# Kernel optimization log

Measured on AMD Instinct MI355X. Metric: run time of the kernel, lower is better.

## Reference

```python
import jax, jax.numpy as jnp
import numpy as np

N_HIDDEN = 14  # number of interior Linear(50,50)+ReLU layers (16 Linears total)
WIDTH = 50
IN_DIM = 16
OUT_DIM = 4
BATCH = 2_000_000


def setup_inputs() -> dict:
    key = jax.random.key(0)
    ks = jax.random.split(key, 7)
    s_in = 1.0 / np.sqrt(IN_DIM)
    s_h = 1.0 / np.sqrt(WIDTH)
    x = jax.random.normal(ks[0], (BATCH, IN_DIM), dtype=jnp.float32)
    W0 = jax.random.uniform(ks[1], (WIDTH, IN_DIM), jnp.float32, -s_in, s_in)
    b0 = jax.random.uniform(ks[2], (WIDTH,), jnp.float32, -s_in, s_in)
    Wh = jax.random.uniform(ks[3], (N_HIDDEN, WIDTH, WIDTH), jnp.float32, -s_h, s_h)
    bh = jax.random.uniform(ks[4], (N_HIDDEN, WIDTH), jnp.float32, -s_h, s_h)
    Wo = jax.random.uniform(ks[5], (OUT_DIM, WIDTH), jnp.float32, -s_h, s_h)
    bo = jax.random.uniform(ks[6], (OUT_DIM,), jnp.float32, -s_h, s_h)
    return {"x": x, "W0": W0, "b0": b0, "Wh": Wh, "bh": bh, "Wo": Wo, "bo": bo}


def reference(x, W0, b0, Wh, bh, Wo, bo):
    # first layer: Linear(in,50) + ReLU   (torch Linear: y = x @ W.T + b)
    h = jax.nn.relu(x @ W0.T + b0)

    # 14 hidden Linear(50,50)+ReLU layers via scan over stacked weights
    def layer(h, wb):
        W, b = wb
        return jax.nn.relu(h @ W.T + b), None

    h, _ = jax.lax.scan(layer, h, (Wh, bh))

    # output layer: Linear(50,out), no activation
    return h @ Wo.T + bo
```

## Files before the change

### kernel.cpp

```cpp
#include <hip/hip_runtime.h>
#include <stdint.h>

#define BATCH 2000000
#define NHID  14
#define NT    6
#define NWAVE 12
#define ROWS_PER_BLOCK (NWAVE * 16 * NT)
#define NTILES ((BATCH + ROWS_PER_BLOCK - 1) / ROWS_PER_BLOCK)
#define NSLOT 118
#define LDS_BYTES (NSLOT * 64 * 16)

typedef float    v4f  __attribute__((ext_vector_type(4)));
typedef _Float16 v8h  __attribute__((ext_vector_type(8)));
typedef __fp16   v2p  __attribute__((ext_vector_type(2)));
typedef uint32_t v4u  __attribute__((ext_vector_type(4)));

__device__ __forceinline__ int kown(int kappa) {
    int s = ((kappa >> 5) << 3) | (kappa & 7);
    int q = (kappa >> 3) & 3;
    return ((s >> 2) << 4) | (q * 4 + (s & 3));
}

__device__ __forceinline__ uint32_t pk(float a, float b) {
    union { v2p v; uint32_t u; } c;
    c.v = __builtin_amdgcn_cvt_pkrtz(a, b);
    return c.u;
}
__device__ __forceinline__ uint32_t relu_pk(float a, float b) {
    v2p z = { (__fp16)0.0f, (__fp16)0.0f };
    union { v2p v; uint32_t u; } c;
    c.v = __builtin_amdgcn_cvt_pkrtz(a, b);
    c.v = __builtin_elementwise_max(c.v, z);
    return c.u;
}

__device__ __forceinline__ void pack2(const v4f* acc, v8h* Bv) {
    union { v4u u; v8h h; } c0, c1;
    c0.u.x = relu_pk(acc[0][0], acc[0][1]);
    c0.u.y = relu_pk(acc[0][2], acc[0][3]);
    c0.u.z = relu_pk(acc[1][0], acc[1][1]);
    c0.u.w = relu_pk(acc[1][2], acc[1][3]);
    c1.u.x = relu_pk(acc[2][0], acc[2][1]);
    c1.u.y = relu_pk(acc[2][2], acc[2][3]);
    c1.u.z = relu_pk(acc[3][0], acc[3][1]);
    c1.u.w = relu_pk(acc[3][2], acc[3][3]);
    Bv[0] = c0.h;
    Bv[1] = c1.h;
}

extern "C" __global__ __launch_bounds__(768, 3)
void mlp16(const float* __restrict__ x,
           const float* __restrict__ W0, const float* __restrict__ b0,
           const float* __restrict__ Wh, const float* __restrict__ bh,
           const float* __restrict__ Wo, const float* __restrict__ bo,
           float* __restrict__ out)
{
    extern __shared__ char smem_raw[];
    v8h* frag = (v8h*)smem_raw;

    const int tid  = threadIdx.x;
    const int lane = tid & 63;
    const int wv   = tid >> 6;
    const int l15  = lane & 15;
    const int quad = lane >> 4;

    for (int s = wv; s < NSLOT; s += NWAVE) {
        float v[8];
        if (s < 4) {
            int m = s * 16 + l15;
            #pragma unroll
            for (int j = 0; j < 8; ++j) {
                int kap = quad * 8 + j;
                float val = 0.f;
                if (kap < 16)      { if (m < 50) val = W0[m * 16 + kap]; }
                else if (kap == 16){ if (m < 50) val = b0[m]; else if (m == 50) val = 1.f; }
                v[j] = val;
            }
        } else if (s < 116) {
            int h = s - 4, l = h >> 3, t = (h >> 2) & 1, mt = h & 3;
            int m = mt * 16 + l15;
            const float* W = Wh + l * 2500;
            #pragma unroll
            for (int j = 0; j < 8; ++j) {
                int ko = kown(t * 32 + quad * 8 + j);
                float val = 0.f;
                if (ko < 50)       { if (m < 50) val = W[m * 50 + ko]; }
                else if (ko == 50) { if (m < 50) val = bh[l * 50 + m]; else if (m == 50) val = 1.f; }
                v[j] = val;
            }
        } else {
            int t = s - 116, m = l15;
            #pragma unroll
            for (int j = 0; j < 8; ++j) {
                int ko = kown(t * 32 + quad * 8 + j);
                float val = 0.f;
                if (m < 4) { if (ko < 50) val = Wo[m * 50 + ko]; else if (ko == 50) val = bo[m]; }
                v[j] = val;
            }
        }
        v8h fv;
        #pragma unroll
        for (int j = 0; j < 8; ++j) fv[j] = (_Float16)v[j];
        frag[s * 64 + lane] = fv;
    }
    __syncthreads();

    const v4f z4 = (v4f){0.f, 0.f, 0.f, 0.f};

    for (int tile = blockIdx.x; tile < NTILES; tile += gridDim.x) {
        const int rowbase = tile * ROWS_PER_BLOCK + wv * (16 * NT);
        v8h Bv[NT][2];

        {
            v8h A0[4];
            #pragma unroll
            for (int mt = 0; mt < 4; ++mt) A0[mt] = frag[mt * 64 + lane];
            #pragma unroll
            for (int nt = 0; nt < NT; ++nt) {
                int r  = rowbase + nt * 16 + l15;
                int rc = r < BATCH ? r : BATCH - 1;
                union { v4u u; v8h h; } bx;
                bx.u = (v4u){0u, 0u, 0u, 0u};
                if (quad < 2) {
                    const float* xp = x + (size_t)rc * 16 + quad * 8;
                    v4f xa = *(const v4f*)xp;
                    v4f xb = *(const v4f*)(xp + 4);
                    bx.u.x = pk(xa[0], xa[1]);
                    bx.u.y = pk(xa[2], xa[3]);
                    bx.u.z = pk(xb[0], xb[1]);
                    bx.u.w = pk(xb[2], xb[3]);
                } else if (quad == 2) {
                    bx.u.x = 0x3C00u;
                }
                v4f acc[4];
                #pragma unroll
                for (int mt = 0; mt < 4; ++mt)
                    acc[mt] = __builtin_amdgcn_mfma_f32_16x16x32_f16(A0[mt], bx.h, z4, 0, 0, 0);
                pack2(acc, Bv[nt]);
            }
        }

        for (int l = 0; l < NHID; ++l) {
            v8h A[2][4];
            const v8h* ab = frag + (4 + l * 8) * 64 + lane;
            #pragma unroll
            for (int t = 0; t < 2; ++t)
                #pragma unroll
                for (int mt = 0; mt < 4; ++mt) A[t][mt] = ab[(t * 4 + mt) * 64];
            #pragma unroll
            for (int nt = 0; nt < NT; ++nt) {
                v4f acc[4];
                #pragma unroll
                for (int mt = 0; mt < 4; ++mt)
                    acc[mt] = __builtin_amdgcn_mfma_f32_16x16x32_f16(A[0][mt], Bv[nt][0], z4, 0, 0, 0);
                #pragma unroll
                for (int mt = 0; mt < 4; ++mt)
                    acc[mt] = __builtin_amdgcn_mfma_f32_16x16x32_f16(A[1][mt], Bv[nt][1], acc[mt], 0, 0, 0);
                pack2(acc, Bv[nt]);
            }
        }

        {
            v8h Ao[2];
            #pragma unroll
            for (int t = 0; t < 2; ++t) Ao[t] = frag[(116 + t) * 64 + lane];
            #pragma unroll
            for (int nt = 0; nt < NT; ++nt) {
                v4f acc = __builtin_amdgcn_mfma_f32_16x16x32_f16(Ao[0], Bv[nt][0], z4, 0, 0, 0);
                acc     = __builtin_amdgcn_mfma_f32_16x16x32_f16(Ao[1], Bv[nt][1], acc, 0, 0, 0);
                int r = rowbase + nt * 16 + l15;
                if (quad == 0 && r < BATCH)
                    *(v4f*)(out + (size_t)r * 4) = acc;
            }
        }
    }
}

extern "C" void kernel_launch(void* const* d_in, const int* in_sizes, int n_in,
                              void* d_out, int out_size, void* d_ws, size_t ws_size,
                              hipStream_t stream)
{
    (void)in_sizes; (void)n_in; (void)d_ws; (void)ws_size; (void)out_size;
    (void)hipFuncSetAttribute(reinterpret_cast<const void*>(mlp16),
                              hipFuncAttributeMaxDynamicSharedMemorySize, LDS_BYTES);
    mlp16<<<256, 768, LDS_BYTES, stream>>>(
        (const float*)d_in[0], (const float*)d_in[1], (const float*)d_in[2],
        (const float*)d_in[3], (const float*)d_in[4], (const float*)d_in[5],
        (const float*)d_in[6], (float*)d_out);
}
```

Baseline: 314.9 us.

## Seed MFMA accumulators with bias and software-pipeline pack with next tile

Folds biases out of the augmented-ones weight column and into a separate LDS table, which is loaded as the initial MFMA accumulator instead of zero. Each layer's loop is restructured with two accumulator sets so the ReLU/fp16 pack of row-tile nt-1 overlaps the MFMAs of tile nt. Rows per wave drop from 6 to 4 tiles, which frees registers for the double-buffered accumulators but makes each weight-fragment load cover fewer rows.

```diff
diff --git a/kernel.cpp b/kernel.cpp
--- a/kernel.cpp
+++ b/kernel.cpp
@@ -3,12 +3,13 @@
 
 #define BATCH 2000000
 #define NHID  14
-#define NT    6
+#define NT    4
 #define NWAVE 12
 #define ROWS_PER_BLOCK (NWAVE * 16 * NT)
 #define NTILES ((BATCH + ROWS_PER_BLOCK - 1) / ROWS_PER_BLOCK)
 #define NSLOT 118
-#define LDS_BYTES (NSLOT * 64 * 16)
+#define BIAS_OFF (NSLOT * 64 * 16)
+#define LDS_BYTES (BIAS_OFF + 16 * 64 * 4)
 
 typedef float    v4f  __attribute__((ext_vector_type(4)));
 typedef _Float16 v8h  __attribute__((ext_vector_type(8)));
@@ -56,7 +57,8 @@
            float* __restrict__ out)
 {
     extern __shared__ char smem_raw[];
-    v8h* frag = (v8h*)smem_raw;
+    v8h*   frag = (v8h*)smem_raw;
+    float* bias = (float*)(smem_raw + BIAS_OFF);
 
     const int tid  = threadIdx.x;
     const int lane = tid & 63;
@@ -71,10 +73,7 @@
             #pragma unroll
             for (int j = 0; j < 8; ++j) {
                 int kap = quad * 8 + j;
-                float val = 0.f;
-                if (kap < 16)      { if (m < 50) val = W0[m * 16 + kap]; }
-                else if (kap == 16){ if (m < 50) val = b0[m]; else if (m == 50) val = 1.f; }
-                v[j] = val;
+                v[j] = (m < 50 && kap < 16) ? W0[m * 16 + kap] : 0.f;
             }
         } else if (s < 116) {
             int h = s - 4, l = h >> 3, t = (h >> 2) & 1, mt = h & 3;
@@ -83,19 +82,14 @@
             #pragma unroll
             for (int j = 0; j < 8; ++j) {
                 int ko = kown(t * 32 + quad * 8 + j);
-                float val = 0.f;
-                if (ko < 50)       { if (m < 50) val = W[m * 50 + ko]; }
-                else if (ko == 50) { if (m < 50) val = bh[l * 50 + m]; else if (m == 50) val = 1.f; }
-                v[j] = val;
+                v[j] = (m < 50 && ko < 50) ? W[m * 50 + ko] : 0.f;
             }
         } else {
             int t = s - 116, m = l15;
             #pragma unroll
             for (int j = 0; j < 8; ++j) {
                 int ko = kown(t * 32 + quad * 8 + j);
-                float val = 0.f;
-                if (m < 4) { if (ko < 50) val = Wo[m * 50 + ko]; else if (ko == 50) val = bo[m]; }
-                v[j] = val;
+                v[j] = (m < 4 && ko < 50) ? Wo[m * 50 + ko] : 0.f;
             }
         }
         v8h fv;
@@ -103,74 +97,101 @@
         for (int j = 0; j < 8; ++j) fv[j] = (_Float16)v[j];
         frag[s * 64 + lane] = fv;
     }
+    for (int i = tid; i < 16 * 64; i += NWAVE * 64) {
+        int l = i >> 6, r = i & 63;
+        float bv = 0.f;
+        if (l == 0)       { if (r < 50) bv = b0[r]; }
+        else if (l <= 14) { if (r < 50) bv = bh[(l - 1) * 50 + r]; }
+        else              { if (r < 4)  bv = bo[r]; }
+        bias[i] = bv;
+    }
     __syncthreads();
-
-    const v4f z4 = (v4f){0.f, 0.f, 0.f, 0.f};
 
     for (int tile = blockIdx.x; tile < NTILES; tile += gridDim.x) {
         const int rowbase = tile * ROWS_PER_BLOCK + wv * (16 * NT);
         v8h Bv[NT][2];
+        v4f acc[2][4];
 
         {
             v8h A0[4];
-            #pragma unroll
-            for (int mt = 0; mt < 4; ++mt) A0[mt] = frag[mt * 64 + lane];
+            v4f bc[4];
+            #pragma unroll
+            for (int mt = 0; mt < 4; ++mt) {
+                A0[mt] = frag[mt * 64 + lane];
+                bc[mt] = *(const v4f*)(bias + 0 * 64 + mt * 16 + quad * 4);
+            }
+            union { v4u u; v8h h; } bx[NT];
             #pragma unroll
             for (int nt = 0; nt < NT; ++nt) {
                 int r  = rowbase + nt * 16 + l15;
                 int rc = r < BATCH ? r : BATCH - 1;
-                union { v4u u; v8h h; } bx;
-                bx.u = (v4u){0u, 0u, 0u, 0u};
+                bx[nt].u = (v4u){0u, 0u, 0u, 0u};
                 if (quad < 2) {
                     const float* xp = x + (size_t)rc * 16 + quad * 8;
                     v4f xa = *(const v4f*)xp;
                     v4f xb = *(const v4f*)(xp + 4);
-                    bx.u.x = pk(xa[0], xa[1]);
-                    bx.u.y = pk(xa[2], xa[3]);
-                    bx.u.z = pk(xb[0], xb[1]);
-                    bx.u.w = pk(xb[2], xb[3]);
-                } else if (quad == 2) {
-                    bx.u.x = 0x3C00u;
+                    bx[nt].u.x = pk(xa[0], xa[1]);
+                    bx[nt].u.y = pk(xa[2], xa[3]);
+                    bx[nt].u.z = pk(xb[0], xb[1]);
+                    bx[nt].u.w = pk(xb[2], xb[3]);
                 }
-                v4f acc[4];
+            }
+            #pragma unroll
+            for (int mt = 0; mt < 4; ++mt)
+                acc[0][mt] = __builtin_amdgcn_mfma_f32_16x16x32_f16(A0[mt], bx[0].h, bc[mt], 0, 0, 0);
+            #pragma unroll
+            for (int nt = 1; nt < NT; ++nt) {
                 #pragma unroll
                 for (int mt = 0; mt < 4; ++mt)
-                    acc[mt] = __builtin_amdgcn_mfma_f32_16x16x32_f16(A0[mt], bx.h, z4, 0, 0, 0);
-                pack2(acc, Bv[nt]);
-            }
+                    acc[nt & 1][mt] = __builtin_amdgcn_mfma_f32_16x16x32_f16(A0[mt], bx[nt].h, bc[mt], 0, 0, 0);
+                pack2(acc[(nt - 1) & 1], Bv[nt - 1]);
+            }
+            pack2(acc[(NT - 1) & 1], Bv[NT - 1]);
         }
 
         for (int l = 0; l < NHID; ++l) {
             v8h A[2][4];
+            v4f bc[4];
             const v8h* ab = frag + (4 + l * 8) * 64 + lane;
             #pragma unroll
             for (int t = 0; t < 2; ++t)
                 #pragma unroll
                 for (int mt = 0; mt < 4; ++mt) A[t][mt] = ab[(t * 4 + mt) * 64];
             #pragma unroll
-            for (int nt = 0; nt < NT; ++nt) {
-                v4f acc[4];
+            for (int mt = 0; mt < 4; ++mt)
+                bc[mt] = *(const v4f*)(bias + (1 + l) * 64 + mt * 16 + quad * 4);
+
+            #pragma unroll
+            for (int mt = 0; mt < 4; ++mt)
+                acc[0][mt] = __builtin_amdgcn_mfma_f32_16x16x32_f16(A[0][mt], Bv[0][0], bc[mt], 0, 0, 0);
+            #pragma unroll
+            for (int mt = 0; mt < 4; ++mt)
+                acc[0][mt] = __builtin_amdgcn_mfma_f32_16x16x32_f16(A[1][mt], Bv[0][1], acc[0][mt], 0, 0, 0);
+            #pragma unroll
+            for (int nt = 1; nt < NT; ++nt) {
                 #pragma unroll
                 for (int mt = 0; mt < 4; ++mt)
-                    acc[mt] = __builtin_amdgcn_mfma_f32_16x16x32_f16(A[0][mt], Bv[nt][0], z4, 0, 0, 0);
+                    acc[nt & 1][mt] = __builtin_amdgcn_mfma_f32_16x16x32_f16(A[0][mt], Bv[nt][0], bc[mt], 0, 0, 0);
                 #pragma unroll
                 for (int mt = 0; mt < 4; ++mt)
-                    acc[mt] = __builtin_amdgcn_mfma_f32_16x16x32_f16(A[1][mt], Bv[nt][1], acc[mt], 0, 0, 0);
-                pack2(acc, Bv[nt]);
-            }
+                    acc[nt & 1][mt] = __builtin_amdgcn_mfma_f32_16x16x32_f16(A[1][mt], Bv[nt][1], acc[nt & 1][mt], 0, 0, 0);
+                pack2(acc[(nt - 1) & 1], Bv[nt - 1]);
+            }
+            pack2(acc[(NT - 1) & 1], Bv[NT - 1]);
         }
 
         {
             v8h Ao[2];
             #pragma unroll
             for (int t = 0; t < 2; ++t) Ao[t] = frag[(116 + t) * 64 + lane];
+            v4f bco = *(const v4f*)(bias + 15 * 64 + quad * 4);
             #pragma unroll
             for (int nt = 0; nt < NT; ++nt) {
-                v4f acc = __builtin_amdgcn_mfma_f32_16x16x32_f16(Ao[0], Bv[nt][0], z4, 0, 0, 0);
-                acc     = __builtin_amdgcn_mfma_f32_16x16x32_f16(Ao[1], Bv[nt][1], acc, 0, 0, 0);
+                v4f a = __builtin_amdgcn_mfma_f32_16x16x32_f16(Ao[0], Bv[nt][0], bco, 0, 0, 0);
+                a     = __builtin_amdgcn_mfma_f32_16x16x32_f16(Ao[1], Bv[nt][1], a, 0, 0, 0);
                 int r = rowbase + nt * 16 + l15;
                 if (quad == 0 && r < BATCH)
-                    *(v4f*)(out + (size_t)r * 4) = acc;
+                    *(v4f*)(out + (size_t)r * 4) = a;
             }
         }
     }
```

Measured after the change: 344.7 us. 9.4% more time.
